# Kernel optimization log

Measured on AMD Instinct MI355X. Metric: run time of the kernel, lower is better.

The kernel has to match this reference:

```python
import jax, jax.numpy as jnp
import numpy as np

N_SYN = 30_000_000
N_POST = 200_000
N_SOURCE = 17_400


def setup_inputs() -> dict:
    key = jax.random.key(0)
    k1, k2, k3, k4 = jax.random.split(key, 4)
    # spike input: ~half of source neurons active (values in {0,1})
    inputs_t = jax.random.randint(k1, (1, N_SOURCE), 0, 2, dtype=jnp.int32)
    # synapse table: col0 = postsynaptic neuron id, col1 = presynaptic source id
    post = jax.random.randint(k2, (N_SYN, 1), 0, N_POST, dtype=jnp.int32)
    pre = jax.random.randint(k3, (N_SYN, 1), 0, N_SOURCE, dtype=jnp.int32)
    indices = jnp.concatenate([post, pre], axis=1)  # [N_SYN, 2]
    weights = jax.random.normal(k4, (N_SYN,), dtype=jnp.float32)
    return {"inputs_t": inputs_t, "indices": indices, "weights": weights, "n_post": N_POST}


def reference(inputs_t, indices, weights, n_post):
    # Original TF code: find active presynaptic columns (inputs_t > 0), gather all
    # synapses whose presynaptic neuron is active (ragged lookup + argsort), then
    # unsorted_segment_sum their weights by postsynaptic id. Mathematically this is:
    #   i_in[post] = sum_{syn : inputs_t[pre[syn]] > 0} weights[syn]
    # which we express as a masked gather + segment_sum (same math, jit-safe).
    active = (inputs_t[0] > 0)                      # [n_source] bool
    pre = indices[:, 1]                             # [n_syn]
    post = indices[:, 0]                            # [n_syn]
    contrib = weights * active[pre].astype(weights.dtype)  # [n_syn]
    i_in = jax.ops.segment_sum(contrib, post, num_segments=n_post)  # [n_post]
    return i_in[None, :]                            # [1, n_post]
```

## Files before the change

### kernel.cpp

```cpp
#include <hip/hip_runtime.h>


typedef int   vint4   __attribute__((ext_vector_type(4)));
typedef float vfloat4 __attribute__((ext_vector_type(4)));
typedef unsigned int uint;

#define P1_BLK    256
#define P1_ITER   8
#define CHUNK     (P1_BLK * P1_ITER * 4)
#define MINICAP   16
#define NB_MAX    392
#define CNTW      ((NB_MAX + 1) / 2)
#define STRIDE_MAX 6272
#define NW_MAX    544
#define P2_BLK    512
#define SPLIT     8
#define NBLK_MAX  3664
#define CBMAX     ((NBLK_MAX + SPLIT - 1) / SPLIT)

__global__ __launch_bounds__(256) void p0_bitmask(
    const int* __restrict__ act, uint* __restrict__ bits_g, int n_src)
{
    int w  = blockIdx.x * blockDim.x + threadIdx.x;
    int nw = (n_src + 31) >> 5;
    if (w < nw) {
        uint m = 0;
        int base = w << 5;
        #pragma unroll
        for (int j = 0; j < 32; ++j) {
            int s = base + j;
            if (s < n_src && act[s] > 0) m |= (1u << j);
        }
        bits_g[w] = m;
    }
}

__global__ __launch_bounds__(P1_BLK, 5) void p1_bucketize(
    const uint* __restrict__ bits_g,
    const vint4* __restrict__ idx4,
    const vfloat4* __restrict__ w4,
    uint* __restrict__ cnt_g,
    uint* __restrict__ pairs_g,
    float* __restrict__ out,
    int sec_base_vec, int sec_nvec, int blocks_s, int nb, int nwords, int stride_dw)
{
    __shared__ uint bits[NW_MAX];
    __shared__ uint cntp[CNTW];
    __shared__ __align__(16) uint ord[STRIDE_MAX];

    const int tid = threadIdx.x;
    for (int i = tid; i < nwords; i += P1_BLK) bits[i] = bits_g[i];
    for (int i = tid; i < CNTW;   i += P1_BLK) cntp[i] = 0;
    __syncthreads();

    const int vbase = sec_base_vec + blockIdx.x * (P1_ITER * P1_BLK);
    const bool full = (vbase - sec_base_vec + P1_ITER * P1_BLK) <= sec_nvec;

    auto process = [&](vint4 pa, vint4 pb, vfloat4 pw) {
        const int   posts[4] = {pa.x, pa.z, pb.x, pb.z};
        const int   pres[4]  = {pa.y, pa.w, pb.y, pb.w};
        const float wsv[4]   = {pw.x, pw.y, pw.z, pw.w};
        #pragma unroll
        for (int j = 0; j < 4; ++j) {
            uint pre = (uint)pres[j];
            if ((bits[pre >> 5] >> (pre & 31u)) & 1u) {
                uint post = (uint)posts[j];
                uint b    = post >> 9;
                uint sh   = (b & 1u) << 4;
                uint r    = (atomicAdd(&cntp[b >> 1], 1u << sh) >> sh) & 0xFFFFu;
                if (r < MINICAP) {
                    uint pk = (__float_as_uint(wsv[j]) & 0xFFFFFE00u) | (post & 511u);
                    ord[(b << 4) + r] = pk;
                } else {
                    atomicAdd(&out[post], wsv[j]);
                }
            }
        }
    };

    if (full) {
        int v = vbase + tid;
        vint4   ia = __builtin_nontemporal_load(&idx4[2 * v]);
        vint4   ib = __builtin_nontemporal_load(&idx4[2 * v + 1]);
        vfloat4 wv = __builtin_nontemporal_load(&w4[v]);
        for (int it = 0; it < P1_ITER - 1; ++it) {
            int vn = v + P1_BLK;
            vint4   na = __builtin_nontemporal_load(&idx4[2 * vn]);
            vint4   nbv = __builtin_nontemporal_load(&idx4[2 * vn + 1]);
            vfloat4 nw = __builtin_nontemporal_load(&w4[vn]);
            process(ia, ib, wv);
            ia = na; ib = nbv; wv = nw; v = vn;
        }
        process(ia, ib, wv);
    } else {
        for (int it = 0; it < P1_ITER; ++it) {
            int v = vbase + it * P1_BLK + tid;
            if ((v - sec_base_vec) < sec_nvec) {
                vint4   ia = __builtin_nontemporal_load(&idx4[2 * v]);
                vint4   ib = __builtin_nontemporal_load(&idx4[2 * v + 1]);
                vfloat4 wv = __builtin_nontemporal_load(&w4[v]);
                process(ia, ib, wv);
            }
        }
    }
    __syncthreads();

    for (int b = tid; b < nb; b += P1_BLK) {
        uint c = (cntp[b >> 1] >> ((b & 1u) << 4)) & 0xFFFFu;
        cnt_g[(size_t)b * (size_t)blocks_s + blockIdx.x] = (c > MINICAP) ? MINICAP : c;
    }
    vint4* dst = (vint4*)(pairs_g + (size_t)blockIdx.x * (size_t)stride_dw);
    const vint4* src = (const vint4*)ord;
    for (int i = tid; i < (stride_dw >> 2); i += P1_BLK)
        dst[i] = src[i];
}

__global__ __launch_bounds__(P2_BLK) void p2_accum(
    const uint* __restrict__ pairs_g,
    const uint* __restrict__ cnt_g,
    float* __restrict__ part,
    int blocks_s, int nb, int stride_dw)
{
    __shared__ float hist[512];
    __shared__ unsigned short cntl[CBMAX];

    const int b   = blockIdx.x;
    const int s   = blockIdx.y;
    const int tid = threadIdx.x;

    const int chunk = (blocks_s + SPLIT - 1) / SPLIT;
    const int blk0  = s * chunk;
    int blkn = blocks_s - blk0;
    if (blkn > chunk) blkn = chunk;
    if (blkn < 0) blkn = 0;

    for (int i = tid; i < 512;  i += P2_BLK) hist[i] = 0.f;
    for (int i = tid; i < blkn; i += P2_BLK)
        cntl[i] = (unsigned short)cnt_g[(size_t)b * (size_t)blocks_s + blk0 + i];
    __syncthreads();

    const int total = blkn << 2;
    const uint boff = ((uint)b) << 4;
    for (int i = tid; i < total; i += P2_BLK) {
        int bl = i >> 2;
        int q  = i & 3;
        const vint4* pv = (const vint4*)(pairs_g
            + (size_t)(blk0 + bl) * (size_t)stride_dw + boff + (uint)(q << 2));
        vint4 pk4 = *pv;
        int c  = (int)cntl[bl];
        int s0 = q << 2;
        const uint pks[4] = {(uint)pk4.x, (uint)pk4.y, (uint)pk4.z, (uint)pk4.w};
        #pragma unroll
        for (int k = 0; k < 4; ++k) {
            if (s0 + k < c)
                atomicAdd(&hist[pks[k] & 511u], __uint_as_float(pks[k] & 0xFFFFFE00u));
        }
    }
    __syncthreads();

    float* dst = part + (size_t)s * ((size_t)nb << 9) + ((size_t)b << 9);
    for (int l = tid; l < 512; l += P2_BLK) dst[l] = hist[l];
}

__global__ __launch_bounds__(256) void p3_merge(
    const float* __restrict__ part, float* __restrict__ out, int n_post, int nb)
{
    int g = blockIdx.x * 256 + threadIdx.x;
    if (g < n_post) {
        size_t span = (size_t)nb << 9;
        float acc = 0.f;
        #pragma unroll
        for (int k = 0; k < SPLIT; ++k) acc += part[(size_t)k * span + g];
        out[g] += acc;
    }
}

__global__ __launch_bounds__(256) void syn_scatter_direct(
    const int* __restrict__ act, const vint4* __restrict__ idx4,
    const vfloat4* __restrict__ w4, float* __restrict__ out, int n_vec)
{
    int t = blockIdx.x * blockDim.x + threadIdx.x;
    if (t >= n_vec) return;
    vint4 ia = idx4[2 * t], ib = idx4[2 * t + 1];
    vfloat4 wv = w4[t];
    if (act[ia.y] > 0) atomicAdd(&out[ia.x], wv.x);
    if (act[ia.w] > 0) atomicAdd(&out[ia.z], wv.y);
    if (act[ib.y] > 0) atomicAdd(&out[ib.x], wv.z);
    if (act[ib.w] > 0) atomicAdd(&out[ib.z], wv.w);
}

extern "C" void kernel_launch(void* const* d_in, const int* in_sizes, int n_in,
                              void* d_out, int out_size, void* d_ws, size_t ws_size,
                              hipStream_t stream) {
    const int*   act     = (const int*)d_in[0];
    const int*   indices = (const int*)d_in[1];
    const float* weights = (const float*)d_in[2];

    const int n_src  = in_sizes[0];
    const int n_syn  = in_sizes[2];
    const int n_post = out_size;
    const int n_vec  = n_syn / 4;

    const int nb        = (n_post + 511) >> 9;
    const int nwords    = (n_src + 31) >> 5;
    const int stride_dw = (nb * MINICAP + 31) & ~31;
    const int nblk_tot  = (n_syn + CHUNK - 1) / CHUNK;

    const size_t parts_bytes   = ((size_t)SPLIT * ((size_t)nb << 9) * 4 + 255) & ~(size_t)255;
    const size_t head_bytes    = 4096 + parts_bytes;
    const size_t per_blk_bytes = (size_t)nb * 4 + (size_t)stride_dw * 4;
    long long nblk_fit = (ws_size > head_bytes)
                       ? (long long)((ws_size - head_bytes) / per_blk_bytes) : 0;

    bool ok = (n_syn % 4 == 0) && (nb <= NB_MAX - 1) && (nwords <= NW_MAX) &&
              (stride_dw <= STRIDE_MAX) && (nblk_tot <= NBLK_MAX) && (nblk_fit >= 1);
    int nsec = ok ? (int)((nblk_tot + nblk_fit - 1) / nblk_fit) : 1000;

    if (!ok || nsec > 8) {
        (void)hipMemsetAsync(d_out, 0, (size_t)n_post * sizeof(float), stream);
        const int grid = (n_vec + 255) / 256;
        syn_scatter_direct<<<grid, 256, 0, stream>>>(
            act, (const vint4*)indices, (const vfloat4*)weights, (float*)d_out, n_vec);
        return;
    }

    const int nblk_s = (nblk_tot + nsec - 1) / nsec;
    uint*  bits_g = (uint*)d_ws;
    float* parts  = (float*)((char*)d_ws + 4096);
    uint*  cnt_g  = (uint*)((char*)d_ws + head_bytes);
    size_t cnt_bytes = ((size_t)nb * (size_t)nblk_s * 4 + 255) & ~(size_t)255;
    uint*  pairs_g = (uint*)((char*)cnt_g + cnt_bytes);

    (void)hipMemsetAsync(d_out, 0, (size_t)n_post * sizeof(float), stream);
    p0_bitmask<<<(nwords + 255) / 256, 256, 0, stream>>>(act, bits_g, n_src);

    const int vec_per_sec = nblk_s * (CHUNK / 4);
    for (int s = 0; s < nsec; ++s) {
        int v0 = s * vec_per_sec;
        int nv = n_vec - v0; if (nv > vec_per_sec) nv = vec_per_sec;
        if (nv <= 0) break;
        int blocks_s = (nv * 4 + CHUNK - 1) / CHUNK;
        p1_bucketize<<<blocks_s, P1_BLK, 0, stream>>>(
            bits_g, (const vint4*)indices, (const vfloat4*)weights,
            cnt_g, pairs_g, (float*)d_out,
            v0, nv, blocks_s, nb, nwords, stride_dw);
        p2_accum<<<dim3(nb, SPLIT), P2_BLK, 0, stream>>>(
            pairs_g, cnt_g, parts, blocks_s, nb, stride_dw);
        p3_merge<<<(n_post + 255) / 256, 256, 0, stream>>>(
            parts, (float*)d_out, n_post, nb);
    }
}
```

Baseline: 487.0 us.

## Drop per-bucket count array by zero-filling slots; pair buckets per p2 block

Phase 1 now zero-fills its shared bucket slot buffer, so unused slots hold zero-weight entries. That removes the global count array and its strided writes. Phase 2 now adds every slot unconditionally and handles two buckets per block with a 1024-entry histogram, with SPLIT raised from 8 to 12 to keep parallelism. The software-pipelined full-block path in phase 1 is also removed and the slot copy-out uses nontemporal stores. Trade-offs: an extra LDS clear per block, atomics on zero values, and more partial sums for the merge to read.

```diff
diff --git a/kernel.cpp b/kernel.cpp
--- a/kernel.cpp
+++ b/kernel.cpp
@@ -10,13 +10,13 @@
 #define CHUNK     (P1_BLK * P1_ITER * 4)
 #define MINICAP   16
 #define NB_MAX    392
+#define NBP_MAX   196
 #define CNTW      ((NB_MAX + 1) / 2)
 #define STRIDE_MAX 6272
 #define NW_MAX    544
 #define P2_BLK    512
-#define SPLIT     8
+#define SPLIT     12
 #define NBLK_MAX  3664
-#define CBMAX     ((NBLK_MAX + SPLIT - 1) / SPLIT)
 
 __global__ __launch_bounds__(256) void p0_bitmask(
     const int* __restrict__ act, uint* __restrict__ bits_g, int n_src)
@@ -39,10 +39,9 @@
     const uint* __restrict__ bits_g,
     const vint4* __restrict__ idx4,
     const vfloat4* __restrict__ w4,
-    uint* __restrict__ cnt_g,
     uint* __restrict__ pairs_g,
     float* __restrict__ out,
-    int sec_base_vec, int sec_nvec, int blocks_s, int nb, int nwords, int stride_dw)
+    int sec_base_vec, int sec_nvec, int nwords, int stride_dw)
 {
     __shared__ uint bits[NW_MAX];
     __shared__ uint cntp[CNTW];
@@ -51,80 +50,60 @@
     const int tid = threadIdx.x;
     for (int i = tid; i < nwords; i += P1_BLK) bits[i] = bits_g[i];
     for (int i = tid; i < CNTW;   i += P1_BLK) cntp[i] = 0;
+    {
+        vint4 z = {0, 0, 0, 0};
+        vint4* o4 = (vint4*)ord;
+        for (int i = tid; i < (stride_dw >> 2); i += P1_BLK) o4[i] = z;
+    }
     __syncthreads();
 
     const int vbase = sec_base_vec + blockIdx.x * (P1_ITER * P1_BLK);
-    const bool full = (vbase - sec_base_vec + P1_ITER * P1_BLK) <= sec_nvec;
-
-    auto process = [&](vint4 pa, vint4 pb, vfloat4 pw) {
-        const int   posts[4] = {pa.x, pa.z, pb.x, pb.z};
-        const int   pres[4]  = {pa.y, pa.w, pb.y, pb.w};
-        const float wsv[4]   = {pw.x, pw.y, pw.z, pw.w};
-        #pragma unroll
-        for (int j = 0; j < 4; ++j) {
-            uint pre = (uint)pres[j];
-            if ((bits[pre >> 5] >> (pre & 31u)) & 1u) {
-                uint post = (uint)posts[j];
-                uint b    = post >> 9;
-                uint sh   = (b & 1u) << 4;
-                uint r    = (atomicAdd(&cntp[b >> 1], 1u << sh) >> sh) & 0xFFFFu;
-                if (r < MINICAP) {
-                    uint pk = (__float_as_uint(wsv[j]) & 0xFFFFFE00u) | (post & 511u);
-                    ord[(b << 4) + r] = pk;
-                } else {
-                    atomicAdd(&out[post], wsv[j]);
+
+    for (int it = 0; it < P1_ITER; ++it) {
+        int v = vbase + it * P1_BLK + tid;
+        if ((v - sec_base_vec) < sec_nvec) {
+            vint4   ia = __builtin_nontemporal_load(&idx4[2 * v]);
+            vint4   ib = __builtin_nontemporal_load(&idx4[2 * v + 1]);
+            vfloat4 wv = __builtin_nontemporal_load(&w4[v]);
+
+            const int   posts[4] = {ia.x, ia.z, ib.x, ib.z};
+            const int   pres[4]  = {ia.y, ia.w, ib.y, ib.w};
+            const float wsv[4]   = {wv.x, wv.y, wv.z, wv.w};
+
+            #pragma unroll
+            for (int j = 0; j < 4; ++j) {
+                uint pre = (uint)pres[j];
+                if ((bits[pre >> 5] >> (pre & 31u)) & 1u) {
+                    uint post = (uint)posts[j];
+                    uint b    = post >> 9;
+                    uint sh   = (b & 1u) << 4;
+                    uint r    = (atomicAdd(&cntp[b >> 1], 1u << sh) >> sh) & 0xFFFFu;
+                    if (r < MINICAP) {
+                        uint pk = (__float_as_uint(wsv[j]) & 0xFFFFFE00u) | (post & 511u);
+                        ord[(b << 4) + r] = pk;
+                    } else {
+                        atomicAdd(&out[post], wsv[j]);
+                    }
                 }
             }
         }
-    };
-
-    if (full) {
-        int v = vbase + tid;
-        vint4   ia = __builtin_nontemporal_load(&idx4[2 * v]);
-        vint4   ib = __builtin_nontemporal_load(&idx4[2 * v + 1]);
-        vfloat4 wv = __builtin_nontemporal_load(&w4[v]);
-        for (int it = 0; it < P1_ITER - 1; ++it) {
-            int vn = v + P1_BLK;
-            vint4   na = __builtin_nontemporal_load(&idx4[2 * vn]);
-            vint4   nbv = __builtin_nontemporal_load(&idx4[2 * vn + 1]);
-            vfloat4 nw = __builtin_nontemporal_load(&w4[vn]);
-            process(ia, ib, wv);
-            ia = na; ib = nbv; wv = nw; v = vn;
-        }
-        process(ia, ib, wv);
-    } else {
-        for (int it = 0; it < P1_ITER; ++it) {
-            int v = vbase + it * P1_BLK + tid;
-            if ((v - sec_base_vec) < sec_nvec) {
-                vint4   ia = __builtin_nontemporal_load(&idx4[2 * v]);
-                vint4   ib = __builtin_nontemporal_load(&idx4[2 * v + 1]);
-                vfloat4 wv = __builtin_nontemporal_load(&w4[v]);
-                process(ia, ib, wv);
-            }
-        }
-    }
-    __syncthreads();
-
-    for (int b = tid; b < nb; b += P1_BLK) {
-        uint c = (cntp[b >> 1] >> ((b & 1u) << 4)) & 0xFFFFu;
-        cnt_g[(size_t)b * (size_t)blocks_s + blockIdx.x] = (c > MINICAP) ? MINICAP : c;
-    }
+    }
+    __syncthreads();
+
     vint4* dst = (vint4*)(pairs_g + (size_t)blockIdx.x * (size_t)stride_dw);
     const vint4* src = (const vint4*)ord;
     for (int i = tid; i < (stride_dw >> 2); i += P1_BLK)
-        dst[i] = src[i];
+        __builtin_nontemporal_store(src[i], &dst[i]);
 }
 
 __global__ __launch_bounds__(P2_BLK) void p2_accum(
     const uint* __restrict__ pairs_g,
-    const uint* __restrict__ cnt_g,
     float* __restrict__ part,
-    int blocks_s, int nb, int stride_dw)
-{
-    __shared__ float hist[512];
-    __shared__ unsigned short cntl[CBMAX];
-
-    const int b   = blockIdx.x;
+    int blocks_s, int nbp, int stride_dw)
+{
+    __shared__ float hist[1024];
+
+    const int bp  = blockIdx.x;
     const int s   = blockIdx.y;
     const int tid = threadIdx.x;
 
@@ -134,40 +113,36 @@
     if (blkn > chunk) blkn = chunk;
     if (blkn < 0) blkn = 0;
 
-    for (int i = tid; i < 512;  i += P2_BLK) hist[i] = 0.f;
-    for (int i = tid; i < blkn; i += P2_BLK)
-        cntl[i] = (unsigned short)cnt_g[(size_t)b * (size_t)blocks_s + blk0 + i];
-    __syncthreads();
-
-    const int total = blkn << 2;
-    const uint boff = ((uint)b) << 4;
+    for (int i = tid; i < 1024; i += P2_BLK) hist[i] = 0.f;
+    __syncthreads();
+
+    const int  total = blkn << 3;
+    const uint boff  = ((uint)bp) << 5;
     for (int i = tid; i < total; i += P2_BLK) {
-        int bl = i >> 2;
-        int q  = i & 3;
+        int bl = i >> 3;
+        int q  = i & 7;
         const vint4* pv = (const vint4*)(pairs_g
             + (size_t)(blk0 + bl) * (size_t)stride_dw + boff + (uint)(q << 2));
         vint4 pk4 = *pv;
-        int c  = (int)cntl[bl];
-        int s0 = q << 2;
+        const uint hi = ((uint)(q >> 2)) << 9;
         const uint pks[4] = {(uint)pk4.x, (uint)pk4.y, (uint)pk4.z, (uint)pk4.w};
         #pragma unroll
-        for (int k = 0; k < 4; ++k) {
-            if (s0 + k < c)
-                atomicAdd(&hist[pks[k] & 511u], __uint_as_float(pks[k] & 0xFFFFFE00u));
-        }
-    }
-    __syncthreads();
-
-    float* dst = part + (size_t)s * ((size_t)nb << 9) + ((size_t)b << 9);
-    for (int l = tid; l < 512; l += P2_BLK) dst[l] = hist[l];
+        for (int k = 0; k < 4; ++k)
+            atomicAdd(&hist[hi | (pks[k] & 511u)],
+                      __uint_as_float(pks[k] & 0xFFFFFE00u));
+    }
+    __syncthreads();
+
+    float* dst = part + (size_t)s * ((size_t)nbp << 10) + ((size_t)bp << 10);
+    for (int l = tid; l < 1024; l += P2_BLK) dst[l] = hist[l];
 }
 
 __global__ __launch_bounds__(256) void p3_merge(
-    const float* __restrict__ part, float* __restrict__ out, int n_post, int nb)
+    const float* __restrict__ part, float* __restrict__ out, int n_post, int nbp)
 {
     int g = blockIdx.x * 256 + threadIdx.x;
     if (g < n_post) {
-        size_t span = (size_t)nb << 9;
+        size_t span = (size_t)nbp << 10;
         float acc = 0.f;
         #pragma unroll
         for (int k = 0; k < SPLIT; ++k) acc += part[(size_t)k * span + g];
@@ -202,18 +177,20 @@
     const int n_vec  = n_syn / 4;
 
     const int nb        = (n_post + 511) >> 9;
+    const int nbp       = (nb + 1) >> 1;
     const int nwords    = (n_src + 31) >> 5;
     const int stride_dw = (nb * MINICAP + 31) & ~31;
     const int nblk_tot  = (n_syn + CHUNK - 1) / CHUNK;
 
-    const size_t parts_bytes   = ((size_t)SPLIT * ((size_t)nb << 9) * 4 + 255) & ~(size_t)255;
+    const size_t parts_bytes   = ((size_t)SPLIT * ((size_t)nbp << 10) * 4 + 255) & ~(size_t)255;
     const size_t head_bytes    = 4096 + parts_bytes;
-    const size_t per_blk_bytes = (size_t)nb * 4 + (size_t)stride_dw * 4;
+    const size_t per_blk_bytes = (size_t)stride_dw * 4;
     long long nblk_fit = (ws_size > head_bytes)
                        ? (long long)((ws_size - head_bytes) / per_blk_bytes) : 0;
 
-    bool ok = (n_syn % 4 == 0) && (nb <= NB_MAX - 1) && (nwords <= NW_MAX) &&
-              (stride_dw <= STRIDE_MAX) && (nblk_tot <= NBLK_MAX) && (nblk_fit >= 1);
+    bool ok = (n_syn % 4 == 0) && (nb <= NB_MAX - 1) && (nbp <= NBP_MAX) &&
+              (nwords <= NW_MAX) && (stride_dw <= STRIDE_MAX) &&
+              (nblk_tot <= NBLK_MAX) && (nblk_fit >= 1);
     int nsec = ok ? (int)((nblk_tot + nblk_fit - 1) / nblk_fit) : 1000;
 
     if (!ok || nsec > 8) {
@@ -225,11 +202,9 @@
     }
 
     const int nblk_s = (nblk_tot + nsec - 1) / nsec;
-    uint*  bits_g = (uint*)d_ws;
-    float* parts  = (float*)((char*)d_ws + 4096);
-    uint*  cnt_g  = (uint*)((char*)d_ws + head_bytes);
-    size_t cnt_bytes = ((size_t)nb * (size_t)nblk_s * 4 + 255) & ~(size_t)255;
-    uint*  pairs_g = (uint*)((char*)cnt_g + cnt_bytes);
+    uint*  bits_g  = (uint*)d_ws;
+    float* parts   = (float*)((char*)d_ws + 4096);
+    uint*  pairs_g = (uint*)((char*)d_ws + head_bytes);
 
     (void)hipMemsetAsync(d_out, 0, (size_t)n_post * sizeof(float), stream);
     p0_bitmask<<<(nwords + 255) / 256, 256, 0, stream>>>(act, bits_g, n_src);
@@ -242,11 +217,10 @@
         int blocks_s = (nv * 4 + CHUNK - 1) / CHUNK;
         p1_bucketize<<<blocks_s, P1_BLK, 0, stream>>>(
             bits_g, (const vint4*)indices, (const vfloat4*)weights,
-            cnt_g, pairs_g, (float*)d_out,
-            v0, nv, blocks_s, nb, nwords, stride_dw);
-        p2_accum<<<dim3(nb, SPLIT), P2_BLK, 0, stream>>>(
-            pairs_g, cnt_g, parts, blocks_s, nb, stride_dw);
+            pairs_g, (float*)d_out, v0, nv, nwords, stride_dw);
+        p2_accum<<<dim3(nbp, SPLIT), P2_BLK, 0, stream>>>(
+            pairs_g, parts, blocks_s, nbp, stride_dw);
         p3_merge<<<(n_post + 255) / 256, 256, 0, stream>>>(
-            parts, (float*)d_out, n_post, nb);
-    }
-}
+            parts, (float*)d_out, n_post, nbp);
+    }
+}
```

Measured after the change: 532.5 us. +9.3%, slower.
